# Kernel tuning notes

Measured on AMD Instinct MI355X. Metric: run time of the kernel, lower is better.

The kernel has to match this reference:

```python
import jax, jax.numpy as jnp
import numpy as np

B, T, D = 2, 2048, 2048
NH, HD, R = 16, 128, 64
CQ, CKV = 1536, 512
WINDOW, CHUNK = 512, 256
MIN_SCALE, MAX_SCALE = 0.5, 2.0
ROPE_BASE = 500000.0
EPS = 1e-6


def setup_inputs() -> dict:
    key = jax.random.key(0)
    ks = jax.random.split(key, 12)
    w = lambda k, shape: (jax.random.normal(k, shape, jnp.float32) * 0.02)
    return {
        "x": jax.random.normal(ks[0], (B, T, D), jnp.float32),
        "uncertainty": jax.random.uniform(ks[1], (B, T), jnp.float32),
        "Wq_down": w(ks[2], (D, CQ)),
        "q_norm_w": jnp.ones((CQ,), jnp.float32),
        "Wq_up": w(ks[3], (CQ, NH * HD)),
        "Wq_rope": w(ks[4], (CQ, NH * R)),
        "Wkv_down": w(ks[5], (D, CKV)),
        "kv_norm_w": jnp.ones((CKV,), jnp.float32),
        "Wk_up": w(ks[6], (CKV, NH * HD)),
        "Wv_up": w(ks[7], (CKV, NH * HD)),
        "Wk_rope": w(ks[8], (D, NH * R)),
        "Wout": w(ks[9], (NH * HD, D)),
        "Wgate": w(ks[10], (D, 1)),
        "bgate": jnp.zeros((1,), jnp.float32),
    }


def rms_norm(x, w):
    return x * jax.lax.rsqrt(jnp.mean(x * x, axis=-1, keepdims=True) + EPS) * w


def epe_cos_sin(positions, uncertainty):
    # freq_idx = arange(r//2)*2/r ; theta = base**(-freq_idx)
    half = R // 2
    freq_idx = jnp.arange(half, dtype=jnp.float32) * 2.0 / R
    theta = ROPE_BASE ** (-freq_idx)                                  # [half]
    scale = MIN_SCALE + jnp.clip(uncertainty, 0.0, 1.0) * (MAX_SCALE - MIN_SCALE)  # [B,T]
    freqs = positions[None, :, None].astype(jnp.float32) * theta[None, None, :] * scale[:, :, None]
    freqs = freqs[:, :, None, :]                                      # [B,T,1,half]
    return jnp.cos(freqs), jnp.sin(freqs)


def apply_rope(x, cos, sin):
    # x: [B,T,nH,r]; rotate halves with per-(B,T) cos/sin broadcast over heads
    half = x.shape[-1] // 2
    x1, x2 = x[..., :half], x[..., half:]
    return jnp.concatenate([x1 * cos - x2 * sin, x2 * cos + x1 * sin], axis=-1)


def sliding_window_attn(Q, K, V, window, chunk):
    # Q,K: [B,nH,T,dk], V: [B,nH,T,dv]; chunked causal sliding-window
    b, nh, t, dk = Q.shape
    dv = V.shape[-1]
    half_w = window // 2
    n_chunks = t // chunk                    # T chosen multiple of chunk
    L = chunk + 2 * half_w
    Kp = jnp.pad(K, ((0, 0), (0, 0), (half_w, half_w), (0, 0)))
    Vp = jnp.pad(V, ((0, 0), (0, 0), (half_w, half_w), (0, 0)))
    starts = jnp.arange(n_chunks) * chunk
    idx = starts[:, None] + jnp.arange(L)[None, :]          # [nC,L] into padded axis
    Kw = Kp[:, :, idx]                                       # [B,nH,nC,L,dk]
    Vw = Vp[:, :, idx]                                       # [B,nH,nC,L,dv]
    Qc = Q.reshape(b, nh, n_chunks, chunk, dk)
    scores = jnp.einsum('bhcqd,bhckd->bhcqk', Qc, Kw) / jnp.sqrt(jnp.float32(dk))
    key_pos = idx - half_w                                   # actual key positions [nC,L]
    q_pos = starts[:, None] + jnp.arange(chunk)[None, :]     # [nC,chunk]
    mask = (key_pos[:, None, :] <= q_pos[:, :, None]) & (key_pos[:, None, :] >= 0)
    scores = jnp.where(mask[None, None], scores, -jnp.inf)
    p = jax.nn.softmax(scores, axis=-1)
    out = jnp.einsum('bhcqk,bhckd->bhcqd', p, Vw)
    return out.reshape(b, nh, t, dv)


def reference(x, uncertainty, Wq_down, q_norm_w, Wq_up, Wq_rope,
              Wkv_down, kv_norm_w, Wk_up, Wv_up, Wk_rope, Wout, Wgate, bgate):
    b, t, d = x.shape
    positions = jnp.arange(t)

    q_lat = rms_norm(x @ Wq_down, q_norm_w)                  # [B,T,CQ]
    q_c = (q_lat @ Wq_up).reshape(b, t, NH, HD)
    q_r = (q_lat @ Wq_rope).reshape(b, t, NH, R)
    kv_lat = rms_norm(x @ Wkv_down, kv_norm_w)               # [B,T,CKV]
    k_c = (kv_lat @ Wk_up).reshape(b, t, NH, HD)
    v = (kv_lat @ Wv_up).reshape(b, t, NH, HD)
    k_r = (x @ Wk_rope).reshape(b, t, NH, R)

    cos, sin = epe_cos_sin(positions, uncertainty)
    q_r = apply_rope(q_r, cos, sin)
    k_r = apply_rope(k_r, cos, sin)

    Q = jnp.concatenate([q_c, q_r], axis=-1).transpose(0, 2, 1, 3)   # [B,nH,T,HD+R]
    K = jnp.concatenate([k_c, k_r], axis=-1).transpose(0, 2, 1, 3)
    V = v.transpose(0, 2, 1, 3)                                       # [B,nH,T,HD]

    out_ar = sliding_window_attn(Q, K, V, WINDOW, CHUNK)

    # full bidirectional SDPA
    scale = 1.0 / jnp.sqrt(jnp.float32(HD + R))
    scores = jnp.einsum('bhqd,bhkd->bhqk', Q, K) * scale
    out_bidir = jnp.einsum('bhqk,bhkd->bhqd', jax.nn.softmax(scores, axis=-1), V)

    alpha = jax.nn.sigmoid((x @ Wgate + bgate)).squeeze(-1)           # [B,T]
    a = alpha[:, None, :, None]
    merged = a * out_bidir + (1.0 - a) * out_ar                       # [B,nH,T,HD]
    merged = merged.transpose(0, 2, 1, 3).reshape(b, t, NH * HD)
    return merged @ Wout, alpha
```

## Files before the change

kernel.cpp:

```cpp
#include <hip/hip_runtime.h>
#include <hip/hip_bf16.h>
#include <math.h>

typedef __hip_bfloat16 bf16;
using v8bf = __attribute__((ext_vector_type(8))) __bf16;
using v4f  = __attribute__((ext_vector_type(4))) float;

#define T_SEQ 2048
#define DMODEL 2048
#define NHEADS 16
#define HDIM 128
#define RDIM 64

__device__ __forceinline__ short f2bfbits(float f) {
  bf16 h = __float2bfloat16(f);
  short s;
  __builtin_memcpy(&s, &h, 2);
  return s;
}

typedef const __attribute__((address_space(1))) unsigned gu32;
typedef __attribute__((address_space(3))) unsigned lu32;
__device__ __forceinline__ void gl_lds16(const void* g, void* l) {
  __builtin_amdgcn_global_load_lds((gu32*)g, (lu32*)l, 16, 0, 0);
}

__global__ void detect_k(const unsigned* __restrict__ x, int* __restrict__ flag) {
  __shared__ int cnt;
  if (threadIdx.x == 0) cnt = 0;
  __syncthreads();
  int c = 0;
#pragma unroll
  for (int i = 0; i < 4; i++) {
    unsigned w = x[threadIdx.x * 4 + i];
    unsigned e = (w >> 7) & 0xFFu;
    if (e < 97u || e > 157u) c++;
  }
  atomicAdd(&cnt, c);
  __syncthreads();
  if (threadIdx.x == 0) flag[0] = (cnt > 256) ? 1 : 0;
}

__global__ __launch_bounds__(256) void conv_all(const void* x_raw,
                                                const void* qnw_raw, const void* kvnw_raw,
                                                const void* wg_raw, const void* bg_raw,
                                                const void* unc_raw,
                                                bf16* xc, bf16* qnw, bf16* kvnw,
                                                bf16* wgc, bf16* bgc, float* uncf,
                                                const int* flag) {
  bool isf = (*flag != 0);
  if (blockIdx.x < 32768) {
    int i = blockIdx.x * 256 + threadIdx.x;
    xc[i] = isf ? __float2bfloat16(((const float*)x_raw)[i]) : ((const bf16*)x_raw)[i];
  } else {
    int i = (blockIdx.x - 32768) * 256 + threadIdx.x;
    if (i < 1536) qnw[i] = isf ? __float2bfloat16(((const float*)qnw_raw)[i]) : ((const bf16*)qnw_raw)[i];
    else if (i < 2048) { int j = i - 1536; kvnw[j] = isf ? __float2bfloat16(((const float*)kvnw_raw)[j]) : ((const bf16*)kvnw_raw)[j]; }
    else if (i < 4096) { int j = i - 2048; wgc[j] = isf ? __float2bfloat16(((const float*)wg_raw)[j]) : ((const bf16*)wg_raw)[j]; }
    else if (i < 4097) bgc[0] = isf ? __float2bfloat16(((const float*)bg_raw)[0]) : ((const bf16*)bg_raw)[0];
    else if (i < 8193) { int j = i - 4097; uncf[j] = isf ? ((const float*)unc_raw)[j] : __bfloat162float(((const bf16*)unc_raw)[j]); }
  }
}

struct TP8 {
  const void* s[8];
  bf16* d[8];
  int rows[8];
  int cols[8];
  int pre[9];
};

__global__ __launch_bounds__(256) void transpose_all(TP8 jobs, const int* __restrict__ flag) {
  __shared__ bf16 tile[32][33];
  int bid = blockIdx.x;
  int w = 0;
#pragma unroll
  for (int k = 0; k < 7; k++) if (bid >= jobs.pre[k + 1]) w = k + 1;
  int lt = bid - jobs.pre[w];
  int rows = jobs.rows[w], cols = jobs.cols[w];
  int tpr = cols >> 5;
  int by = (lt / tpr) << 5, bx = (lt % tpr) << 5;
  const void* src = jobs.s[w];
  bf16* dst = jobs.d[w];
  int tx = threadIdx.x & 31, ty = threadIdx.x >> 5;
  bool isf = (*flag != 0);
#pragma unroll
  for (int i = 0; i < 32; i += 8) {
    size_t idx = (size_t)(by + ty + i) * cols + bx + tx;
    tile[ty + i][tx] = isf ? __float2bfloat16(((const float*)src)[idx])
                           : ((const bf16*)src)[idx];
  }
  __syncthreads();
#pragma unroll
  for (int i = 0; i < 32; i += 8)
    dst[(size_t)(bx + ty + i) * rows + by + tx] = tile[tx][ty + i];
}

__global__ __launch_bounds__(256) void transpose_str(const bf16* __restrict__ src,
                                                     bf16* __restrict__ dst,
                                                     int srcStride, int dstStride) {
  __shared__ bf16 tile[32][33];
  int bx = blockIdx.x * 32, by = blockIdx.y * 32;
  int tx = threadIdx.x & 31, ty = threadIdx.x >> 5;
#pragma unroll
  for (int i = 0; i < 32; i += 8)
    tile[ty + i][tx] = src[(size_t)(by + ty + i) * srcStride + bx + tx];
  __syncthreads();
#pragma unroll
  for (int i = 0; i < 32; i += 8)
    dst[(size_t)(bx + ty + i) * dstStride + by + tx] = tile[tx][ty + i];
}

__global__ __launch_bounds__(256) void gemm_tn(const bf16* __restrict__ A,
                                               const bf16* __restrict__ BT,
                                               bf16* __restrict__ Cb,
                                               int M, int N, int K,
                                               const int* __restrict__ oflag,
                                               void* __restrict__ dvout) {
  __shared__ __align__(16) short lsa[128 * 32];
  __shared__ __align__(16) short lsb[128 * 32];
  const int m0 = blockIdx.y * 128, n0 = blockIdx.x * 128;
  const int tid = threadIdx.x;
  const int w = tid >> 6, lane = tid & 63, quad = lane >> 4, l16 = lane & 15;
  const int wm = (w >> 1) * 64, wn = (w & 1) * 64;
  const int srow = ((lane >> 5) & 1) * 8 + (lane & 7);
  const int skq  = (lane >> 3) & 3;
  const int r0 = w * 2, r1 = w * 2 + 1;
  const bf16* Ab0 = A  + (size_t)(m0 + r0 * 16 + srow) * K + skq * 8;
  const bf16* Ab1 = A  + (size_t)(m0 + r1 * 16 + srow) * K + skq * 8;
  const bf16* Bb0 = BT + (size_t)(n0 + r0 * 16 + srow) * K + skq * 8;
  const bf16* Bb1 = BT + (size_t)(n0 + r1 * 16 + srow) * K + skq * 8;
  short* la0 = &lsa[r0 * 512];
  short* la1 = &lsa[r1 * 512];
  short* lb0 = &lsb[r0 * 512];
  short* lb1 = &lsb[r1 * 512];

  v4f acc[4][4];
#pragma unroll
  for (int i = 0; i < 4; i++)
#pragma unroll
    for (int j = 0; j < 4; j++) acc[i][j] = (v4f){0.f, 0.f, 0.f, 0.f};

  for (int kb = 0; kb < K; kb += 32) {
    __syncthreads();
    gl_lds16(Ab0 + kb, la0);
    gl_lds16(Ab1 + kb, la1);
    gl_lds16(Bb0 + kb, lb0);
    gl_lds16(Bb1 + kb, lb1);
    __syncthreads();

    v8bf af[4], bfr[4];
#pragma unroll
    for (int i = 0; i < 4; i++) {
      int row = wm + i * 16 + l16;
      af[i] = *reinterpret_cast<const v8bf*>(
          &lsa[((row >> 3) << 8) + (quad << 6) + ((row & 7) << 3)]);
    }
#pragma unroll
    for (int j = 0; j < 4; j++) {
      int row = wn + j * 16 + l16;
      bfr[j] = *reinterpret_cast<const v8bf*>(
          &lsb[((row >> 3) << 8) + (quad << 6) + ((row & 7) << 3)]);
    }
#pragma unroll
    for (int i = 0; i < 4; i++)
#pragma unroll
      for (int j = 0; j < 4; j++)
        acc[i][j] = __builtin_amdgcn_mfma_f32_16x16x32_bf16(af[i], bfr[j], acc[i][j], 0, 0, 0);
  }
  const bool isf = dvout && (*oflag != 0);
#pragma unroll
  for (int i = 0; i < 4; i++)
#pragma unroll
    for (int j = 0; j < 4; j++)
#pragma unroll
      for (int r = 0; r < 4; r++) {
        int row = m0 + wm + i * 16 + quad * 4 + r;
        int col = n0 + wn + j * 16 + l16;
        float vv = acc[i][j][r];
        size_t idx = (size_t)row * N + col;
        if (dvout) {
          if (isf) ((float*)dvout)[idx] = vv;
          else     ((bf16*)dvout)[idx] = __float2bfloat16(vv);
        } else {
          Cb[idx] = __float2bfloat16(vv);
        }
      }
}

__global__ __launch_bounds__(256) void rmsnorm_both(const bf16* __restrict__ xproj,
                                                    const bf16* __restrict__ qnw,
                                                    const bf16* __restrict__ kvnw,
                                                    bf16* __restrict__ q_lat,
                                                    bf16* __restrict__ kv_lat) {
  int bid = blockIdx.x, tid = threadIdx.x;
  bool isq = bid < 4096;
  int row = isq ? bid : bid - 4096;
  int C = isq ? 1536 : 512;
  const bf16* r = xproj + (size_t)row * 3072 + (isq ? 0 : 1536);
  const bf16* w = isq ? qnw : kvnw;
  bf16* o = (isq ? q_lat : kv_lat) + (size_t)row * C;
  float s = 0.f;
  for (int i = tid; i < C; i += 256) { float v = __bfloat162float(r[i]); s += v * v; }
#pragma unroll
  for (int m = 32; m; m >>= 1) s += __shfl_xor(s, m);
  __shared__ float red[4];
  if ((tid & 63) == 0) red[tid >> 6] = s;
  __syncthreads();
  float tot = red[0] + red[1] + red[2] + red[3];
  float rs = rsqrtf(tot / (float)C + 1e-6f);
  for (int i = tid; i < C; i += 256)
    o[i] = __float2bfloat16(__bfloat162float(r[i]) * rs * __bfloat162float(w[i]));
}

__global__ __launch_bounds__(256) void rope_gate(bf16* __restrict__ qcr,
                                                 bf16* __restrict__ xproj,
                                                 const float* __restrict__ unc,
                                                 const bf16* __restrict__ x,
                                                 const bf16* __restrict__ wg,
                                                 const bf16* __restrict__ bg,
                                                 float* __restrict__ af,
                                                 void* __restrict__ dout,
                                                 const int* __restrict__ flag) {
  __shared__ float red[4];
  int tid = threadIdx.x;
  if (blockIdx.x < 8192) {
    int idx = blockIdx.x * 256 + tid;
    int j = idx & 31, h = (idx >> 5) & 15, bt = idx >> 9;
    int t = bt & (T_SEQ - 1);
    float u = unc[bt];
    u = fminf(fmaxf(u, 0.f), 1.f);
    float scale = 0.5f + 1.5f * u;
    float theta = expf(-(float)j * (1.f / 32.f) * logf(500000.f));
    float f = (float)t * theta * scale;
    float c = cosf(f), s = sinf(f);
    size_t base = (size_t)bt * 3072 + 2048 + h * RDIM + j;
    {
      float x1 = __bfloat162float(qcr[base]), x2 = __bfloat162float(qcr[base + 32]);
      qcr[base]      = __float2bfloat16(x1 * c - x2 * s);
      qcr[base + 32] = __float2bfloat16(x2 * c + x1 * s);
    }
    {
      float x1 = __bfloat162float(xproj[base]), x2 = __bfloat162float(xproj[base + 32]);
      xproj[base]      = __float2bfloat16(x1 * c - x2 * s);
      xproj[base + 32] = __float2bfloat16(x2 * c + x1 * s);
    }
  } else {
    int row = blockIdx.x - 8192;
    const bf16* xr = x + (size_t)row * DMODEL;
    float s = 0.f;
    for (int i = tid; i < DMODEL; i += 256)
      s += __bfloat162float(xr[i]) * __bfloat162float(wg[i]);
#pragma unroll
    for (int m = 32; m; m >>= 1) s += __shfl_xor(s, m);
    if ((tid & 63) == 0) red[tid >> 6] = s;
    __syncthreads();
    if (tid == 0) {
      float tot = red[0] + red[1] + red[2] + red[3] + __bfloat162float(bg[0]);
      float a = 1.f / (1.f + expf(-tot));
      af[row] = a;
      size_t oi = (size_t)8388608 + row;
      if (*flag) ((float*)dout)[oi] = a;
      else       ((bf16*)dout)[oi] = __float2bfloat16(a);
    }
  }
}

template <int IS_AR>
__global__ __launch_bounds__(512) void attn_k(const bf16* __restrict__ qcr,
                                              const bf16* __restrict__ kcv,
                                              const bf16* __restrict__ xproj,
                                              const bf16* __restrict__ vt,
                                              const bf16* __restrict__ ob,
                                              const float* __restrict__ alphaF,
                                              bf16* __restrict__ out) {
  constexpr int LDK = 200;
  constexpr int LDV = 72;
  constexpr int LDP = 72;
  __shared__ __align__(16) short lk[64 * LDK];
  __shared__ __align__(16) short lvt[128 * LDV];
  __shared__ __align__(16) short lp[8 * 16 * LDP];

  const int b = blockIdx.z, h = blockIdx.y, qt = blockIdx.x;
  const int qs = qt * 128;
  const int tid = threadIdx.x;
  const int w = tid >> 6, lane = tid & 63, quad = lane >> 4, l16 = lane & 15;
  const int q0 = qs + w * 16;

  v8bf qf[6];
  {
    int qrow = q0 + l16;
    const bf16* qcb = qcr + ((size_t)b * T_SEQ + qrow) * 3072 + h * HDIM;
#pragma unroll
    for (int s_ = 0; s_ < 4; s_++)
      qf[s_] = *reinterpret_cast<const v8bf*>(qcb + s_ * 32 + quad * 8);
    const bf16* qrb = qcr + ((size_t)b * T_SEQ + qrow) * 3072 + 2048 + h * RDIM;
#pragma unroll
    for (int s_ = 0; s_ < 2; s_++)
      qf[4 + s_] = *reinterpret_cast<const v8bf*>(qrb + s_ * 32 + quad * 8);
  }

  float l_lane[4] = {0.f, 0.f, 0.f, 0.f};
  v4f oacc[8];
#pragma unroll
  for (int i = 0; i < 8; i++) oacc[i] = (v4f){0.f, 0.f, 0.f, 0.f};

  int klo = 0, khi = T_SEQ;
  if (IS_AR) {
    int c = qs >> 8;
    klo = (c > 0) ? (c * 256 - 256) : 0;
    khi = qs + 128;
  }
  const float sc = 0.07216878364870323f;
  short* pw = &lp[w * 16 * LDP];

  for (int kb = klo; kb < khi; kb += 64) {
    __syncthreads();
#pragma unroll
    for (int i = 0; i < 3; i++) {
      int c = i * 512 + tid;
      int row = c / 24, dg = c % 24;
      int key = kb + row;
      const bf16* src;
      if (dg < 16) src = kcv + ((size_t)b * T_SEQ + key) * 4096 + h * HDIM + dg * 8;
      else         src = xproj + ((size_t)b * T_SEQ + key) * 3072 + 2048 + h * RDIM + (dg - 16) * 8;
      *reinterpret_cast<v8bf*>(&lk[row * LDK + dg * 8]) = *reinterpret_cast<const v8bf*>(src);
    }
#pragma unroll
    for (int i = 0; i < 2; i++) {
      int c = i * 512 + tid;
      int d = c >> 3, kg = c & 7;
      *reinterpret_cast<v8bf*>(&lvt[d * LDV + kg * 8]) =
          *reinterpret_cast<const v8bf*>(vt + (size_t)(h * HDIM + d) * (2 * T_SEQ) + b * T_SEQ + kb + kg * 8);
    }
    __syncthreads();

    const bool wactive = !IS_AR || (kb <= q0 + 15);
    if (wactive) {
      float pnew[4][4];
#pragma unroll
      for (int j = 0; j < 4; j++) {
        const bool jact = !IS_AR || (kb + j * 16 <= q0 + 15);
        if (jact) {
          v4f a = (v4f){0.f, 0.f, 0.f, 0.f};
#pragma unroll
          for (int s_ = 0; s_ < 6; s_++) {
            v8bf kf = *reinterpret_cast<const v8bf*>(&lk[(j * 16 + l16) * LDK + s_ * 32 + quad * 8]);
            a = __builtin_amdgcn_mfma_f32_16x16x32_bf16(qf[s_], kf, a, 0, 0, 0);
          }
#pragma unroll
          for (int r = 0; r < 4; r++) {
            float p = __expf(a[r] * sc);
            if (IS_AR) {
              int k = kb + j * 16 + l16;
              int q = q0 + quad * 4 + r;
              p = (k <= q) ? p : 0.f;
            }
            pnew[r][j] = p;
            l_lane[r] += p;
          }
        } else {
#pragma unroll
          for (int r = 0; r < 4; r++) pnew[r][j] = 0.f;
        }
      }
#pragma unroll
      for (int r = 0; r < 4; r++) {
        int prow = quad * 4 + r;
#pragma unroll
        for (int j = 0; j < 4; j++)
          pw[prow * LDP + j * 16 + l16] = f2bfbits(pnew[r][j]);
      }
      asm volatile("s_waitcnt lgkmcnt(0)" ::: "memory");
      v8bf pf[2];
#pragma unroll
      for (int st = 0; st < 2; st++)
        pf[st] = *reinterpret_cast<const v8bf*>(&pw[l16 * LDP + st * 32 + quad * 8]);
#pragma unroll
      for (int nd = 0; nd < 8; nd++) {
#pragma unroll
        for (int st = 0; st < 2; st++) {
          v8bf vf = *reinterpret_cast<const v8bf*>(&lvt[(nd * 16 + l16) * LDV + st * 32 + quad * 8]);
          oacc[nd] = __builtin_amdgcn_mfma_f32_16x16x32_bf16(pf[st], vf, oacc[nd], 0, 0, 0);
        }
      }
    }
  }

#pragma unroll
  for (int r = 0; r < 4; r++) {
    float l = l_lane[r];
#pragma unroll
    for (int m = 1; m < 16; m <<= 1) l += __shfl_xor(l, m);
    float inv = 1.f / l;
    int q = q0 + quad * 4 + r;
    size_t base = ((size_t)b * T_SEQ + q) * DMODEL + h * HDIM;
    if (IS_AR) {
      float a = alphaF[b * T_SEQ + q];
#pragma unroll
      for (int nd = 0; nd < 8; nd++) {
        float vb = __bfloat162float(ob[base + nd * 16 + l16]);
        out[base + nd * 16 + l16] = __float2bfloat16(a * vb + (1.f - a) * (oacc[nd][r] * inv));
      }
    } else {
#pragma unroll
      for (int nd = 0; nd < 8; nd++)
        out[base + nd * 16 + l16] = __float2bfloat16(oacc[nd][r] * inv);
    }
  }
}

extern "C" void kernel_launch(void* const* d_in, const int* in_sizes, int n_in,
                              void* d_out, int out_size, void* d_ws, size_t ws_size,
                              hipStream_t stream) {
  const void* x_raw    = d_in[0];
  const void* unc_raw  = d_in[1];
  const void* Wqd_raw  = d_in[2];
  const void* qnw_raw  = d_in[3];
  const void* Wqu_raw  = d_in[4];
  const void* Wqr_raw  = d_in[5];
  const void* Wkvd_raw = d_in[6];
  const void* kvnw_raw = d_in[7];
  const void* Wku_raw  = d_in[8];
  const void* Wvu_raw  = d_in[9];
  const void* Wkr_raw  = d_in[10];
  const void* Wo_raw   = d_in[11];
  const void* Wg_raw   = d_in[12];
  const void* bg_raw   = d_in[13];

  char* ws = (char*)d_ws;
  size_t off = 0;
  auto alloc = [&](size_t bytes) -> void* {
    char* p = ws + off;
    off += (bytes + 255) & ~(size_t)255;
    return p;
  };
  int*  flag   = (int*)alloc(256);
  bf16* xc     = (bf16*)alloc((size_t)4096 * 2048 * 2);
  float* uncf  = (float*)alloc((size_t)4096 * 4);
  bf16* qnw    = (bf16*)alloc(1536 * 2);
  bf16* kvnw   = (bf16*)alloc(512 * 2);
  bf16* wgc    = (bf16*)alloc(2048 * 2);
  bf16* bgc    = (bf16*)alloc(256);
  bf16* BT1    = (bf16*)alloc((size_t)3072 * 2048 * 2);
  bf16* BT2    = (bf16*)alloc((size_t)3072 * 1536 * 2);
  bf16* BT3    = (bf16*)alloc((size_t)4096 * 512 * 2);
  bf16* WoT    = (bf16*)alloc((size_t)2048 * 2048 * 2);
  bf16* xproj  = (bf16*)alloc((size_t)4096 * 3072 * 2);
  bf16* q_lat  = (bf16*)alloc((size_t)4096 * 1536 * 2);
  bf16* kv_lat = (bf16*)alloc((size_t)4096 * 512 * 2);
  bf16* qcr    = (bf16*)alloc((size_t)4096 * 3072 * 2);
  bf16* kcv    = (bf16*)alloc((size_t)4096 * 4096 * 2);
  bf16* vT     = (bf16*)alloc((size_t)4096 * 2048 * 2);
  bf16* out_b  = (bf16*)alloc((size_t)4096 * 2048 * 2);
  bf16* attno  = (bf16*)alloc((size_t)4096 * 2048 * 2);
  float* alphaF= (float*)alloc((size_t)4096 * 4);

  detect_k<<<1, 256, 0, stream>>>((const unsigned*)x_raw, flag);

  conv_all<<<32801, 256, 0, stream>>>(x_raw, qnw_raw, kvnw_raw, Wg_raw, bg_raw, unc_raw,
                                      xc, qnw, kvnw, wgc, bgc, uncf, flag);

  TP8 jobs;
  const void* srcs[8] = {Wqd_raw, Wkvd_raw, Wkr_raw, Wqu_raw, Wqr_raw, Wku_raw, Wvu_raw, Wo_raw};
  bf16* dsts[8] = {BT1, BT1 + (size_t)1536 * 2048, BT1 + (size_t)2048 * 2048,
                   BT2, BT2 + (size_t)2048 * 1536,
                   BT3, BT3 + (size_t)2048 * 512, WoT};
  int rws[8] = {2048, 2048, 2048, 1536, 1536, 512, 512, 2048};
  int cls[8] = {1536, 512, 1024, 2048, 1024, 2048, 2048, 2048};
  int acc_t = 0;
  for (int i = 0; i < 8; i++) {
    jobs.s[i] = srcs[i]; jobs.d[i] = dsts[i];
    jobs.rows[i] = rws[i]; jobs.cols[i] = cls[i];
    jobs.pre[i] = acc_t;
    acc_t += (rws[i] / 32) * (cls[i] / 32);
  }
  jobs.pre[8] = acc_t;
  transpose_all<<<acc_t, 256, 0, stream>>>(jobs, flag);

  auto gemmb = [&](const bf16* A, const bf16* BT, bf16* C, int M, int N, int K) {
    gemm_tn<<<dim3(N / 128, M / 128), 256, 0, stream>>>(A, BT, C, M, N, K, nullptr, nullptr);
  };

  gemmb(xc, BT1, xproj, 4096, 3072, 2048);
  rmsnorm_both<<<8192, 256, 0, stream>>>(xproj, qnw, kvnw, q_lat, kv_lat);
  gemmb(q_lat, BT2, qcr, 4096, 3072, 1536);
  gemmb(kv_lat, BT3, kcv, 4096, 4096, 512);

  transpose_str<<<dim3(64, 128), 256, 0, stream>>>(kcv + 2048, vT, 4096, 4096);

  rope_gate<<<12288, 256, 0, stream>>>(qcr, xproj, uncf, xc, wgc, bgc, alphaF, d_out, flag);

  attn_k<0><<<dim3(16, 16, 2), 512, 0, stream>>>(qcr, kcv, xproj, vT, nullptr, nullptr, out_b);
  attn_k<1><<<dim3(16, 16, 2), 512, 0, stream>>>(qcr, kcv, xproj, vT, out_b, alphaF, attno);

  gemm_tn<<<dim3(16, 32), 256, 0, stream>>>(attno, WoT, nullptr, 4096, 2048, 2048, flag, d_out);

  (void)in_sizes; (void)n_in; (void)out_size; (void)ws_size;
}
```

Before: 683.6 us.

## Rewrite attention with 32x32 MFMA, register P via permlane swap, LDS-staged output

Rewrites the attention kernel so each wave handles 32 query rows using 32x32x16 bf16 MFMA, computing S transposed (K times Q) so the softmax probabilities can be repacked into B-operand fragments in registers with v_permlane32_swap, removing the LDS round-trip for P. Blocks shrink to 256 threads with launch bounds allowing two blocks per CU, and the LDS buffers are merged. Output is staged through LDS so global stores and the AR merge read use 16-byte vector accesses. It also raises wave priority around the MFMA section. This trades more registers per wave (larger Q fragments and accumulators) for fewer LDS operations and better MFMA efficiency.

```diff
diff --git a/kernel.cpp b/kernel.cpp
--- a/kernel.cpp
+++ b/kernel.cpp
@@ -5,6 +5,10 @@
 typedef __hip_bfloat16 bf16;
 using v8bf = __attribute__((ext_vector_type(8))) __bf16;
 using v4f  = __attribute__((ext_vector_type(4))) float;
+using f32x16 = __attribute__((ext_vector_type(16))) float;
+using v4u = __attribute__((ext_vector_type(4))) unsigned;
+using v4s = __attribute__((ext_vector_type(4))) short;
+using v8s = __attribute__((ext_vector_type(8))) short;
 
 #define T_SEQ 2048
 #define DMODEL 2048
@@ -17,6 +21,18 @@
   short s;
   __builtin_memcpy(&s, &h, 2);
   return s;
+}
+
+__device__ __forceinline__ float bfbits2f(short s) {
+  bf16 h;
+  __builtin_memcpy(&h, &s, 2);
+  return __bfloat162float(h);
+}
+
+__device__ __forceinline__ unsigned pk2bf(float a, float b) {
+  unsigned lo = (unsigned short)f2bfbits(a);
+  unsigned hi = (unsigned short)f2bfbits(b);
+  return lo | (hi << 16);
 }
 
 typedef const __attribute__((address_space(1))) unsigned gu32;
@@ -267,43 +283,45 @@
 }
 
 template <int IS_AR>
-__global__ __launch_bounds__(512) void attn_k(const bf16* __restrict__ qcr,
-                                              const bf16* __restrict__ kcv,
-                                              const bf16* __restrict__ xproj,
-                                              const bf16* __restrict__ vt,
-                                              const bf16* __restrict__ ob,
-                                              const float* __restrict__ alphaF,
-                                              bf16* __restrict__ out) {
+__global__ __launch_bounds__(256, 2) void attn_k(const bf16* __restrict__ qcr,
+                                                 const bf16* __restrict__ kcv,
+                                                 const bf16* __restrict__ xproj,
+                                                 const bf16* __restrict__ vt,
+                                                 const bf16* __restrict__ ob,
+                                                 const float* __restrict__ alphaF,
+                                                 bf16* __restrict__ out) {
   constexpr int LDK = 200;
   constexpr int LDV = 72;
-  constexpr int LDP = 72;
-  __shared__ __align__(16) short lk[64 * LDK];
-  __shared__ __align__(16) short lvt[128 * LDV];
-  __shared__ __align__(16) short lp[8 * 16 * LDP];
+  __shared__ __align__(16) short sh[64 * LDK + 128 * LDV];
+  short* lk  = sh;
+  short* lvt = sh + 64 * LDK;
 
   const int b = blockIdx.z, h = blockIdx.y, qt = blockIdx.x;
   const int qs = qt * 128;
   const int tid = threadIdx.x;
-  const int w = tid >> 6, lane = tid & 63, quad = lane >> 4, l16 = lane & 15;
-  const int q0 = qs + w * 16;
-
-  v8bf qf[6];
+  const int w = tid >> 6, lane = tid & 63;
+  const int l5 = lane & 31, h8 = lane >> 5;
+  const int q0 = qs + w * 32;
+  const int myq = q0 + l5;
+
+  v8bf qf[12];
   {
-    int qrow = q0 + l16;
-    const bf16* qcb = qcr + ((size_t)b * T_SEQ + qrow) * 3072 + h * HDIM;
-#pragma unroll
-    for (int s_ = 0; s_ < 4; s_++)
-      qf[s_] = *reinterpret_cast<const v8bf*>(qcb + s_ * 32 + quad * 8);
-    const bf16* qrb = qcr + ((size_t)b * T_SEQ + qrow) * 3072 + 2048 + h * RDIM;
-#pragma unroll
-    for (int s_ = 0; s_ < 2; s_++)
-      qf[4 + s_] = *reinterpret_cast<const v8bf*>(qrb + s_ * 32 + quad * 8);
-  }
-
-  float l_lane[4] = {0.f, 0.f, 0.f, 0.f};
-  v4f oacc[8];
-#pragma unroll
-  for (int i = 0; i < 8; i++) oacc[i] = (v4f){0.f, 0.f, 0.f, 0.f};
+    const bf16* qcb = qcr + ((size_t)b * T_SEQ + myq) * 3072 + h * HDIM;
+#pragma unroll
+    for (int ks = 0; ks < 8; ks++)
+      qf[ks] = *reinterpret_cast<const v8bf*>(qcb + ks * 16 + h8 * 8);
+    const bf16* qrb = qcr + ((size_t)b * T_SEQ + myq) * 3072 + 2048 + h * RDIM;
+#pragma unroll
+    for (int ks = 0; ks < 4; ks++)
+      qf[8 + ks] = *reinterpret_cast<const v8bf*>(qrb + ks * 16 + h8 * 8);
+  }
+
+  float l_sum = 0.f;
+  f32x16 oacc[4];
+#pragma unroll
+  for (int nd = 0; nd < 4; nd++)
+#pragma unroll
+    for (int r = 0; r < 16; r++) oacc[nd][r] = 0.f;
 
   int klo = 0, khi = T_SEQ;
   if (IS_AR) {
@@ -312,100 +330,117 @@
     khi = qs + 128;
   }
   const float sc = 0.07216878364870323f;
-  short* pw = &lp[w * 16 * LDP];
 
   for (int kb = klo; kb < khi; kb += 64) {
     __syncthreads();
 #pragma unroll
-    for (int i = 0; i < 3; i++) {
-      int c = i * 512 + tid;
-      int row = c / 24, dg = c % 24;
+    for (int i = 0; i < 6; i++) {
+      int c = i * 256 + tid;
+      int row = c / 24, dg = c - row * 24;
       int key = kb + row;
-      const bf16* src;
-      if (dg < 16) src = kcv + ((size_t)b * T_SEQ + key) * 4096 + h * HDIM + dg * 8;
-      else         src = xproj + ((size_t)b * T_SEQ + key) * 3072 + 2048 + h * RDIM + (dg - 16) * 8;
+      const bf16* src = (dg < 16)
+          ? kcv + ((size_t)b * T_SEQ + key) * 4096 + h * HDIM + dg * 8
+          : xproj + ((size_t)b * T_SEQ + key) * 3072 + 2048 + h * RDIM + (dg - 16) * 8;
       *reinterpret_cast<v8bf*>(&lk[row * LDK + dg * 8]) = *reinterpret_cast<const v8bf*>(src);
     }
 #pragma unroll
-    for (int i = 0; i < 2; i++) {
-      int c = i * 512 + tid;
+    for (int i = 0; i < 4; i++) {
+      int c = i * 256 + tid;
       int d = c >> 3, kg = c & 7;
       *reinterpret_cast<v8bf*>(&lvt[d * LDV + kg * 8]) =
           *reinterpret_cast<const v8bf*>(vt + (size_t)(h * HDIM + d) * (2 * T_SEQ) + b * T_SEQ + kb + kg * 8);
     }
     __syncthreads();
 
-    const bool wactive = !IS_AR || (kb <= q0 + 15);
-    if (wactive) {
-      float pnew[4][4];
-#pragma unroll
-      for (int j = 0; j < 4; j++) {
-        const bool jact = !IS_AR || (kb + j * 16 <= q0 + 15);
-        if (jact) {
-          v4f a = (v4f){0.f, 0.f, 0.f, 0.f};
-#pragma unroll
-          for (int s_ = 0; s_ < 6; s_++) {
-            v8bf kf = *reinterpret_cast<const v8bf*>(&lk[(j * 16 + l16) * LDK + s_ * 32 + quad * 8]);
-            a = __builtin_amdgcn_mfma_f32_16x16x32_bf16(qf[s_], kf, a, 0, 0, 0);
+    if (IS_AR && kb > q0 + 31) continue;
+
+    __builtin_amdgcn_s_setprio(1);
+    v8bf pfrag[4];
+#pragma unroll
+    for (int j = 0; j < 2; j++) {
+      bool jact = !IS_AR || (kb + j * 32 <= q0 + 31);
+      if (jact) {
+        f32x16 s;
+#pragma unroll
+        for (int r = 0; r < 16; r++) s[r] = 0.f;
+#pragma unroll
+        for (int ks = 0; ks < 12; ks++) {
+          v8bf kf = *reinterpret_cast<const v8bf*>(&lk[(j * 32 + l5) * LDK + ks * 16 + h8 * 8]);
+          s = __builtin_amdgcn_mfma_f32_32x32x16_bf16(kf, qf[ks], s, 0, 0, 0);
+        }
+        float p[16];
+#pragma unroll
+        for (int r = 0; r < 16; r++) {
+          float e = __expf(s[r] * sc);
+          if (IS_AR) {
+            int k = kb + j * 32 + (r & 3) + 8 * (r >> 2) + 4 * h8;
+            e = (k <= myq) ? e : 0.f;
           }
-#pragma unroll
-          for (int r = 0; r < 4; r++) {
-            float p = __expf(a[r] * sc);
-            if (IS_AR) {
-              int k = kb + j * 16 + l16;
-              int q = q0 + quad * 4 + r;
-              p = (k <= q) ? p : 0.f;
-            }
-            pnew[r][j] = p;
-            l_lane[r] += p;
-          }
-        } else {
-#pragma unroll
-          for (int r = 0; r < 4; r++) pnew[r][j] = 0.f;
+          p[r] = e;
+          l_sum += e;
+        }
+#pragma unroll
+        for (int cc = 0; cc < 2; cc++) {
+          unsigned Y0 = pk2bf(p[cc * 8 + 0], p[cc * 8 + 1]);
+          unsigned Y1 = pk2bf(p[cc * 8 + 2], p[cc * 8 + 3]);
+          unsigned Y2 = pk2bf(p[cc * 8 + 4], p[cc * 8 + 5]);
+          unsigned Y3 = pk2bf(p[cc * 8 + 6], p[cc * 8 + 7]);
+          asm volatile("v_permlane32_swap_b32 %0, %1" : "+v"(Y0), "+v"(Y2));
+          asm volatile("v_permlane32_swap_b32 %0, %1" : "+v"(Y1), "+v"(Y3));
+          v4u t; t.x = Y0; t.y = Y1; t.z = Y2; t.w = Y3;
+          pfrag[j * 2 + cc] = __builtin_bit_cast(v8bf, t);
+        }
+      } else {
+#pragma unroll
+        for (int cc = 0; cc < 2; cc++) {
+          v4u t; t.x = 0; t.y = 0; t.z = 0; t.w = 0;
+          pfrag[j * 2 + cc] = __builtin_bit_cast(v8bf, t);
         }
       }
-#pragma unroll
-      for (int r = 0; r < 4; r++) {
-        int prow = quad * 4 + r;
-#pragma unroll
-        for (int j = 0; j < 4; j++)
-          pw[prow * LDP + j * 16 + l16] = f2bfbits(pnew[r][j]);
+    }
+#pragma unroll
+    for (int ck = 0; ck < 4; ck++) {
+#pragma unroll
+      for (int nd = 0; nd < 4; nd++) {
+        v8bf vf = *reinterpret_cast<const v8bf*>(&lvt[(nd * 32 + l5) * LDV + ck * 16 + h8 * 8]);
+        oacc[nd] = __builtin_amdgcn_mfma_f32_32x32x16_bf16(vf, pfrag[ck], oacc[nd], 0, 0, 0);
       }
-      asm volatile("s_waitcnt lgkmcnt(0)" ::: "memory");
-      v8bf pf[2];
-#pragma unroll
-      for (int st = 0; st < 2; st++)
-        pf[st] = *reinterpret_cast<const v8bf*>(&pw[l16 * LDP + st * 32 + quad * 8]);
-#pragma unroll
-      for (int nd = 0; nd < 8; nd++) {
-#pragma unroll
-        for (int st = 0; st < 2; st++) {
-          v8bf vf = *reinterpret_cast<const v8bf*>(&lvt[(nd * 16 + l16) * LDV + st * 32 + quad * 8]);
-          oacc[nd] = __builtin_amdgcn_mfma_f32_16x16x32_bf16(pf[st], vf, oacc[nd], 0, 0, 0);
-        }
-      }
-    }
-  }
-
-#pragma unroll
-  for (int r = 0; r < 4; r++) {
-    float l = l_lane[r];
-#pragma unroll
-    for (int m = 1; m < 16; m <<= 1) l += __shfl_xor(l, m);
-    float inv = 1.f / l;
-    int q = q0 + quad * 4 + r;
-    size_t base = ((size_t)b * T_SEQ + q) * DMODEL + h * HDIM;
+    }
+    __builtin_amdgcn_s_setprio(0);
+  }
+
+  l_sum += __shfl_xor(l_sum, 32);
+  float inv = 1.f / l_sum;
+
+  __syncthreads();
+  short* tile = sh + w * (32 * 136);
+#pragma unroll
+  for (int nd = 0; nd < 4; nd++)
+#pragma unroll
+    for (int rg = 0; rg < 4; rg++) {
+      v4s pk;
+#pragma unroll
+      for (int i = 0; i < 4; i++) pk[i] = f2bfbits(oacc[nd][rg * 4 + i] * inv);
+      *reinterpret_cast<v4s*>(&tile[l5 * 136 + nd * 32 + rg * 8 + h8 * 4]) = pk;
+    }
+  __syncthreads();
+#pragma unroll
+  for (int i = 0; i < 8; i++) {
+    int r = i * 4 + (lane >> 4);
+    int q2 = q0 + r;
+    int dcol = (lane & 15) * 8;
+    v8s mv = *reinterpret_cast<const v8s*>(&tile[r * 136 + dcol]);
+    size_t gbase = ((size_t)b * T_SEQ + q2) * DMODEL + h * HDIM + dcol;
     if (IS_AR) {
-      float a = alphaF[b * T_SEQ + q];
-#pragma unroll
-      for (int nd = 0; nd < 8; nd++) {
-        float vb = __bfloat162float(ob[base + nd * 16 + l16]);
-        out[base + nd * 16 + l16] = __float2bfloat16(a * vb + (1.f - a) * (oacc[nd][r] * inv));
-      }
+      float a = alphaF[b * T_SEQ + q2];
+      v8s ov = *reinterpret_cast<const v8s*>((const void*)(ob + gbase));
+      v8s res;
+#pragma unroll
+      for (int e = 0; e < 8; e++)
+        res[e] = f2bfbits(a * bfbits2f(ov[e]) + (1.f - a) * bfbits2f(mv[e]));
+      *reinterpret_cast<v8s*>((void*)(out + gbase)) = res;
     } else {
-#pragma unroll
-      for (int nd = 0; nd < 8; nd++)
-        out[base + nd * 16 + l16] = __float2bfloat16(oacc[nd][r] * inv);
+      *reinterpret_cast<v8s*>((void*)(out + gbase)) = mv;
     }
   }
 }
@@ -491,8 +526,8 @@
 
   rope_gate<<<12288, 256, 0, stream>>>(qcr, xproj, uncf, xc, wgc, bgc, alphaF, d_out, flag);
 
-  attn_k<0><<<dim3(16, 16, 2), 512, 0, stream>>>(qcr, kcv, xproj, vT, nullptr, nullptr, out_b);
-  attn_k<1><<<dim3(16, 16, 2), 512, 0, stream>>>(qcr, kcv, xproj, vT, out_b, alphaF, attno);
+  attn_k<0><<<dim3(16, 16, 2), 256, 0, stream>>>(qcr, kcv, xproj, vT, nullptr, nullptr, out_b);
+  attn_k<1><<<dim3(16, 16, 2), 256, 0, stream>>>(qcr, kcv, xproj, vT, out_b, alphaF, attno);
 
   gemm_tn<<<dim3(16, 32), 256, 0, stream>>>(attno, WoT, nullptr, 4096, 2048, 2048, flag, d_out);
 
```

Result: no change. 674.8 us (-1.3%).
